# Kernel tuning notes

Measured on AMD Instinct MI355X. Metric: run time of the kernel, lower is better.

The kernel has to match this reference:

```python
import jax, jax.numpy as jnp
import numpy as np

TOP_K = 2


def setup_inputs() -> dict:
    key = jax.random.key(0)
    k1, k2 = jax.random.split(key)
    x = jax.random.normal(k1, (4, 4096, 2048), dtype=jnp.float32)
    W = jax.random.normal(k2, (64, 2048), dtype=jnp.float32) * (1.0 / np.sqrt(2048))
    return {"x": x, "W": W}


def reference(x, W):
    B, S, D = x.shape
    E = W.shape[0]
    # logits: [B*S, E] via linear router (no bias)
    flat = x.reshape(-1, D)
    logits = jnp.einsum('td,ed->te', flat, W)
    probs = jax.nn.softmax(logits, axis=-1)
    # eval path: top-k indices
    _, top_k_indices = jax.lax.top_k(probs, TOP_K)          # [T, K]
    # scatter 1s -> mask; scatter gathered probs -> router_probs (== probs*mask)
    router_mask = jax.nn.one_hot(top_k_indices, E, dtype=probs.dtype).sum(axis=-2)  # [T, E]
    router_probs = probs * router_mask
    # normalize (top_k > 1: gradient flows through the sum)
    router_probs = router_probs / router_probs.sum(axis=-1, keepdims=True)
    return (router_mask.reshape(B, S, E),
            top_k_indices.reshape(B, S, TOP_K),
            router_probs.reshape(B, S, E),
            probs.reshape(B, S, E))
```

## Files before the change

kernel.cpp:

```cpp
#include <hip/hip_runtime.h>
#include <math.h>


#define D_DIM 2048
#define E_DIM 64

typedef __bf16 bf16x8 __attribute__((ext_vector_type(8)));
typedef unsigned short us8 __attribute__((ext_vector_type(8)));
typedef float f32x4 __attribute__((ext_vector_type(4)));

static __device__ __forceinline__ unsigned short f2bf(float f) {
    unsigned int u = __float_as_uint(f);
    u += 0x7fffu + ((u >> 16) & 1u);
    return (unsigned short)(u >> 16);
}
static __device__ __forceinline__ float bf2f(unsigned short h) {
    return __uint_as_float(((unsigned int)h) << 16);
}
static __device__ __forceinline__ void split4(const float4 v, ushort4* h, ushort4* l) {
    h->x = f2bf(v.x); l->x = f2bf(v.x - bf2f(h->x));
    h->y = f2bf(v.y); l->y = f2bf(v.y - bf2f(h->y));
    h->z = f2bf(v.z); l->z = f2bf(v.z - bf2f(h->z));
    h->w = f2bf(v.w); l->w = f2bf(v.w - bf2f(h->w));
}

__global__ __launch_bounds__(256, 1) void convert_w(
    const float4* __restrict__ W4, unsigned short* __restrict__ WH,
    unsigned short* __restrict__ WL)
{
    int i = blockIdx.x * 256 + threadIdx.x;
    float4 v = W4[i];
    ushort4 h, l;
    split4(v, &h, &l);
    *(ushort4*)&WH[i * 4] = h;
    *(ushort4*)&WL[i * 4] = l;
}

__global__ __launch_bounds__(256, 4) void router_fused(
    const float* __restrict__ x,
    const unsigned short* __restrict__ WHg, const unsigned short* __restrict__ WLg,
    float* __restrict__ mask_out, float* __restrict__ idx_out,
    float* __restrict__ rp_out, float* __restrict__ probs_out)
{
    __shared__ __align__(16) float Lp[4][16 * 64];

    const int tid  = threadIdx.x;
    const int lane = tid & 63;
    const int wv   = tid >> 6;
    const int quad = lane >> 4;
    const int l16  = lane & 15;
    const int t0   = blockIdx.x << 4;

    const int k0 = wv << 9;

    const float*          xp  = x   + (size_t)(t0 + l16) * D_DIM + k0 + quad * 8;
    const unsigned short* whp = WHg + (size_t)l16 * D_DIM + k0 + quad * 8;
    const unsigned short* wlp = WLg + (size_t)l16 * D_DIM + k0 + quad * 8;

    f32x4 acc[4];
    #pragma unroll
    for (int n = 0; n < 4; ++n) { f32x4 z = {0.f, 0.f, 0.f, 0.f}; acc[n] = z; }

    #pragma unroll 2
    for (int j = 0; j < 16; ++j) {
        const int o = j << 5;
        float4 xa = *(const float4*)(xp + o);
        float4 xb = *(const float4*)(xp + o + 4);
        ushort4 h0, l0, h1, l1;
        split4(xa, &h0, &l0);
        split4(xb, &h1, &l1);
        union { us8 u; bf16x8 b; } ua, ul;
        ua.u = (us8){h0.x, h0.y, h0.z, h0.w, h1.x, h1.y, h1.z, h1.w};
        ul.u = (us8){l0.x, l0.y, l0.z, l0.w, l1.x, l1.y, l1.z, l1.w};

        #pragma unroll
        for (int n = 0; n < 4; ++n) {
            bf16x8 bh = *(const bf16x8*)(whp + n * 16 * D_DIM + o);
            bf16x8 bl = *(const bf16x8*)(wlp + n * 16 * D_DIM + o);
            acc[n] = __builtin_amdgcn_mfma_f32_16x16x32_bf16(ua.b, bh, acc[n], 0, 0, 0);
            acc[n] = __builtin_amdgcn_mfma_f32_16x16x32_bf16(ul.b, bh, acc[n], 0, 0, 0);
            acc[n] = __builtin_amdgcn_mfma_f32_16x16x32_bf16(ua.b, bl, acc[n], 0, 0, 0);
        }
    }

    #pragma unroll
    for (int n = 0; n < 4; ++n)
        #pragma unroll
        for (int r = 0; r < 4; ++r)
            Lp[wv][(quad * 4 + r) * 64 + n * 16 + l16] = acc[n][r];
    __syncthreads();

    for (int i = 0; i < 4; ++i) {
        const int tl = wv * 4 + i;
        const int t  = t0 + tl;
        const float v = Lp[0][tl * 64 + lane] + Lp[1][tl * 64 + lane]
                      + Lp[2][tl * 64 + lane] + Lp[3][tl * 64 + lane];

        float bv = v; int bi = lane;
        #pragma unroll
        for (int off = 1; off < 64; off <<= 1) {
            float ov = __shfl_xor(bv, off, 64);
            int   oi = __shfl_xor(bi, off, 64);
            bool take = (ov > bv) || (ov == bv && oi < bi);
            bv = take ? ov : bv;
            bi = take ? oi : bi;
        }
        const float m = bv; const int i1 = bi;

        const float p = __expf(v - m);
        float s = p;
        #pragma unroll
        for (int off = 1; off < 64; off <<= 1) s += __shfl_xor(s, off, 64);
        const float prob = p / s;

        const float v2 = (lane == i1) ? -INFINITY : v;
        float cv = v2; int ci = lane;
        #pragma unroll
        for (int off = 1; off < 64; off <<= 1) {
            float ov = __shfl_xor(cv, off, 64);
            int   oi = __shfl_xor(ci, off, 64);
            bool take = (ov > cv) || (ov == cv && oi < ci);
            cv = take ? ov : cv;
            ci = take ? oi : ci;
        }
        const int i2 = ci;

        const float pd = __shfl(prob, i1, 64) + __shfl(prob, i2, 64);
        const bool top = (lane == i1) || (lane == i2);

        const size_t base = (size_t)t * 64 + lane;
        mask_out[base]  = top ? 1.f : 0.f;
        rp_out[base]    = top ? prob / pd : 0.f;
        probs_out[base] = prob;
        if (lane == 0) {
            idx_out[(size_t)t * 2]     = (float)i1;
            idx_out[(size_t)t * 2 + 1] = (float)i2;
        }
    }
}

extern "C" void kernel_launch(void* const* d_in, const int* in_sizes, int n_in,
                              void* d_out, int out_size, void* d_ws, size_t ws_size,
                              hipStream_t stream) {
    const float* x = (const float*)d_in[0];
    const float* W = (const float*)d_in[1];
    float* out = (float*)d_out;

    const int T  = in_sizes[0] / D_DIM;
    const int WN = in_sizes[1];

    unsigned short* WH = (unsigned short*)d_ws;
    unsigned short* WL = WH + WN;

    float* mask_out  = out;
    float* idx_out   = out + (size_t)T * E_DIM;
    float* rp_out    = idx_out + (size_t)T * 2;
    float* probs_out = rp_out + (size_t)T * E_DIM;

    convert_w<<<dim3(WN / 1024), dim3(256), 0, stream>>>((const float4*)W, WH, WL);
    router_fused<<<dim3(T / 16), dim3(256), 0, stream>>>(
        x, WH, WL, mask_out, idx_out, rp_out, probs_out);
}
```

Baseline: 248.5 us.

## Replace split-bf16 MFMA router GEMM with direct FP32 FMA over 64-token blocks

The router logits are now computed with plain FP32 fused multiply-adds straight from the original weights. This drops the separate weight-conversion kernel and the three-MFMA hi/lo bf16 split emulation. Each block has 1024 threads and covers 64 tokens: waves split the experts into four groups of 16 and the K dimension into four chunks of 512. Weight reads are wave-uniform so they can go through scalar loads, and the partial sums are reduced through padded shared memory. The trade is giving up matrix-core throughput for exact FP32 arithmetic and less conversion work, at the cost of x loads strided by a full row across lanes.

```diff
diff --git a/kernel.cpp b/kernel.cpp
--- a/kernel.cpp
+++ b/kernel.cpp
@@ -5,96 +5,56 @@
 #define D_DIM 2048
 #define E_DIM 64
 
-typedef __bf16 bf16x8 __attribute__((ext_vector_type(8)));
-typedef unsigned short us8 __attribute__((ext_vector_type(8)));
-typedef float f32x4 __attribute__((ext_vector_type(4)));
-
-static __device__ __forceinline__ unsigned short f2bf(float f) {
-    unsigned int u = __float_as_uint(f);
-    u += 0x7fffu + ((u >> 16) & 1u);
-    return (unsigned short)(u >> 16);
-}
-static __device__ __forceinline__ float bf2f(unsigned short h) {
-    return __uint_as_float(((unsigned int)h) << 16);
-}
-static __device__ __forceinline__ void split4(const float4 v, ushort4* h, ushort4* l) {
-    h->x = f2bf(v.x); l->x = f2bf(v.x - bf2f(h->x));
-    h->y = f2bf(v.y); l->y = f2bf(v.y - bf2f(h->y));
-    h->z = f2bf(v.z); l->z = f2bf(v.z - bf2f(h->z));
-    h->w = f2bf(v.w); l->w = f2bf(v.w - bf2f(h->w));
-}
-
-__global__ __launch_bounds__(256, 1) void convert_w(
-    const float4* __restrict__ W4, unsigned short* __restrict__ WH,
-    unsigned short* __restrict__ WL)
-{
-    int i = blockIdx.x * 256 + threadIdx.x;
-    float4 v = W4[i];
-    ushort4 h, l;
-    split4(v, &h, &l);
-    *(ushort4*)&WH[i * 4] = h;
-    *(ushort4*)&WL[i * 4] = l;
-}
-
-__global__ __launch_bounds__(256, 4) void router_fused(
-    const float* __restrict__ x,
-    const unsigned short* __restrict__ WHg, const unsigned short* __restrict__ WLg,
+__global__ __launch_bounds__(1024, 4) void router_fused(
+    const float* __restrict__ x, const float* __restrict__ Wg,
     float* __restrict__ mask_out, float* __restrict__ idx_out,
     float* __restrict__ rp_out, float* __restrict__ probs_out)
 {
-    __shared__ __align__(16) float Lp[4][16 * 64];
+    __shared__ __align__(16) float Lp[4][64][68];
 
     const int tid  = threadIdx.x;
     const int lane = tid & 63;
     const int wv   = tid >> 6;
-    const int quad = lane >> 4;
-    const int l16  = lane & 15;
-    const int t0   = blockIdx.x << 4;
 
-    const int k0 = wv << 9;
+    const int t0 = blockIdx.x << 6;
 
-    const float*          xp  = x   + (size_t)(t0 + l16) * D_DIM + k0 + quad * 8;
-    const unsigned short* whp = WHg + (size_t)l16 * D_DIM + k0 + quad * 8;
-    const unsigned short* wlp = WLg + (size_t)l16 * D_DIM + k0 + quad * 8;
+    const int eq = __builtin_amdgcn_readfirstlane(wv >> 2);
+    const int kq = __builtin_amdgcn_readfirstlane(wv & 3);
 
-    f32x4 acc[4];
+    const float* xq = x  + (size_t)(t0 + lane) * D_DIM + kq * 512;
+    const float* Wq = Wg + (size_t)(eq * 16) * D_DIM + kq * 512;
+
+    float acc[16];
     #pragma unroll
-    for (int n = 0; n < 4; ++n) { f32x4 z = {0.f, 0.f, 0.f, 0.f}; acc[n] = z; }
+    for (int e = 0; e < 16; ++e) acc[e] = 0.f;
 
-    #pragma unroll 2
-    for (int j = 0; j < 16; ++j) {
-        const int o = j << 5;
-        float4 xa = *(const float4*)(xp + o);
-        float4 xb = *(const float4*)(xp + o + 4);
-        ushort4 h0, l0, h1, l1;
-        split4(xa, &h0, &l0);
-        split4(xb, &h1, &l1);
-        union { us8 u; bf16x8 b; } ua, ul;
-        ua.u = (us8){h0.x, h0.y, h0.z, h0.w, h1.x, h1.y, h1.z, h1.w};
-        ul.u = (us8){l0.x, l0.y, l0.z, l0.w, l1.x, l1.y, l1.z, l1.w};
-
+    for (int j = 0; j < 512; j += 4) {
+        const float4 xv = *(const float4*)(xq + j);
         #pragma unroll
-        for (int n = 0; n < 4; ++n) {
-            bf16x8 bh = *(const bf16x8*)(whp + n * 16 * D_DIM + o);
-            bf16x8 bl = *(const bf16x8*)(wlp + n * 16 * D_DIM + o);
-            acc[n] = __builtin_amdgcn_mfma_f32_16x16x32_bf16(ua.b, bh, acc[n], 0, 0, 0);
-            acc[n] = __builtin_amdgcn_mfma_f32_16x16x32_bf16(ul.b, bh, acc[n], 0, 0, 0);
-            acc[n] = __builtin_amdgcn_mfma_f32_16x16x32_bf16(ua.b, bl, acc[n], 0, 0, 0);
+        for (int e = 0; e < 16; ++e) {
+            const float* wp = Wq + e * D_DIM + j;
+            float a = acc[e];
+            a = fmaf(xv.x, wp[0], a);
+            a = fmaf(xv.y, wp[1], a);
+            a = fmaf(xv.z, wp[2], a);
+            a = fmaf(xv.w, wp[3], a);
+            acc[e] = a;
         }
     }
 
     #pragma unroll
-    for (int n = 0; n < 4; ++n)
-        #pragma unroll
-        for (int r = 0; r < 4; ++r)
-            Lp[wv][(quad * 4 + r) * 64 + n * 16 + l16] = acc[n][r];
+    for (int e = 0; e < 16; e += 4) {
+        float4 v4 = make_float4(acc[e], acc[e + 1], acc[e + 2], acc[e + 3]);
+        *(float4*)&Lp[kq][lane][eq * 16 + e] = v4;
+    }
     __syncthreads();
 
+    #pragma unroll
     for (int i = 0; i < 4; ++i) {
         const int tl = wv * 4 + i;
         const int t  = t0 + tl;
-        const float v = Lp[0][tl * 64 + lane] + Lp[1][tl * 64 + lane]
-                      + Lp[2][tl * 64 + lane] + Lp[3][tl * 64 + lane];
+        const float v = Lp[0][tl][lane] + Lp[1][tl][lane]
+                      + Lp[2][tl][lane] + Lp[3][tl][lane];
 
         float bv = v; int bi = lane;
         #pragma unroll
@@ -146,18 +106,13 @@
     const float* W = (const float*)d_in[1];
     float* out = (float*)d_out;
 
-    const int T  = in_sizes[0] / D_DIM;
-    const int WN = in_sizes[1];
-
-    unsigned short* WH = (unsigned short*)d_ws;
-    unsigned short* WL = WH + WN;
+    const int T = in_sizes[0] / D_DIM;
 
     float* mask_out  = out;
     float* idx_out   = out + (size_t)T * E_DIM;
     float* rp_out    = idx_out + (size_t)T * 2;
     float* probs_out = rp_out + (size_t)T * E_DIM;
 
-    convert_w<<<dim3(WN / 1024), dim3(256), 0, stream>>>((const float4*)W, WH, WL);
-    router_fused<<<dim3(T / 16), dim3(256), 0, stream>>>(
-        x, WH, WL, mask_out, idx_out, rp_out, probs_out);
+    router_fused<<<dim3(T / 64), dim3(1024), 0, stream>>>(
+        x, W, mask_out, idx_out, rp_out, probs_out);
 }
```

After: 386.1 us. +55.3%, slower.
